# Kernel optimization log

Measured on AMD Instinct MI355X. Metric: run time of the kernel, lower is better.

Reference implementation:

```python
import jax, jax.numpy as jnp
import numpy as np

IN_F, OUT_F, R = 4096, 4096, 16
ALPHA = 32.0
SCALING = ALPHA / R


def setup_inputs() -> dict:
    key = jax.random.key(0)
    kx, kw, ka = jax.random.split(key, 3)
    x = jax.random.normal(kx, (4, 2048, IN_F), dtype=jnp.float32)
    # xavier_normal for weight: std = sqrt(2/(fan_in+fan_out))
    std = float(np.sqrt(2.0 / (IN_F + OUT_F)))
    weight = jax.random.normal(kw, (OUT_F, IN_F), dtype=jnp.float32) * std
    bias = jnp.zeros((OUT_F,), dtype=jnp.float32)
    A = jax.random.normal(ka, (R, IN_F), dtype=jnp.float32) * 0.01
    # B initialized to zeros in the module, but use small random values so the
    # LoRA path is numerically exercised for kernel correctness testing.
    B = jax.random.normal(jax.random.fold_in(key, 7), (OUT_F, R), dtype=jnp.float32) * 0.01
    return {"x": x, "weight": weight, "bias": bias, "A": A, "B": B}


def reference(x, weight, bias, A, B):
    # out = x @ W^T + bias + scaling * ((x @ A^T) @ B^T)
    out = jnp.einsum('bsi,oi->bso', x, weight) + bias
    xa = jnp.einsum('bsi,ri->bsr', x, A)           # [b, s, r] low-rank projection
    out = out + SCALING * jnp.einsum('bsr,or->bso', xa, B)
    return out
```

## Files before the change

kernel.cpp:

```cpp
#include <hip/hip_runtime.h>
#include <hip/hip_bf16.h>
#include <cstdint>
#include <cstddef>


#define IN_F   4096
#define OUT_F  4096
#define MROWS  8192
#define RLORA  16
#define LORA_SCALE 2.0f

#define BM 128
#define BN 128
#define BK 32

typedef __bf16 bf16x8 __attribute__((ext_vector_type(8)));
typedef float  f32x4  __attribute__((ext_vector_type(4)));


__device__ __forceinline__ unsigned short f2bf_rne(float f) {
    union { float f; unsigned u; } v; v.f = f;
    unsigned u = v.u;
    return (unsigned short)((u + 0x7FFFu + ((u >> 16) & 1u)) >> 16);
}

__device__ __forceinline__ void gl_lds16(const unsigned short* g, unsigned short* l) {
    __builtin_amdgcn_global_load_lds(
        (const __attribute__((address_space(1))) unsigned int*)g,
        (__attribute__((address_space(3))) unsigned int*)l,
        16, 0, 0);
}


__global__ void cast_x_kernel(const float* __restrict__ x,
                              unsigned short* __restrict__ xb) {
    int i = blockIdx.x * blockDim.x + threadIdx.x;
    float4 v = ((const float4*)x)[i];
    ushort4 o;
    o.x = f2bf_rne(v.x); o.y = f2bf_rne(v.y);
    o.z = f2bf_rne(v.z); o.w = f2bf_rne(v.w);
    ((ushort4*)xb)[i] = o;
}


__global__ void fold_w_kernel(const float* __restrict__ W,
                              const float* __restrict__ A,
                              const float* __restrict__ B,
                              unsigned short* __restrict__ Wp) {
    int o = blockIdx.x;
    __shared__ float sB[RLORA];
    if (threadIdx.x < RLORA) sB[threadIdx.x] = B[o * RLORA + threadIdx.x];
    __syncthreads();
    const float4* W4  = (const float4*)(W + (size_t)o * IN_F);
    ushort4*      Wp4 = (ushort4*)(Wp + (size_t)o * IN_F);
    for (int i4 = threadIdx.x; i4 < IN_F / 4; i4 += blockDim.x) {
        float4 w = W4[i4];
        float ax = 0.f, ay = 0.f, az = 0.f, aw = 0.f;
        #pragma unroll
        for (int r = 0; r < RLORA; ++r) {
            float4 a = ((const float4*)(A + (size_t)r * IN_F))[i4];
            float s = sB[r];
            ax += s * a.x; ay += s * a.y; az += s * a.z; aw += s * a.w;
        }
        w.x += LORA_SCALE * ax; w.y += LORA_SCALE * ay;
        w.z += LORA_SCALE * az; w.w += LORA_SCALE * aw;
        ushort4 ov;
        ov.x = f2bf_rne(w.x); ov.y = f2bf_rne(w.y);
        ov.z = f2bf_rne(w.z); ov.w = f2bf_rne(w.w);
        Wp4[i4] = ov;
    }
}


__global__ __launch_bounds__(256)
void gemm_bt_bias(const unsigned short* __restrict__ Xb,
                  const unsigned short* __restrict__ Wb,
                  const float* __restrict__ bias,
                  float* __restrict__ out) {
    __shared__ __align__(16) unsigned short As[BM * BK];
    __shared__ __align__(16) unsigned short Bs[BN * BK];

    const int tid  = threadIdx.x;
    const int wave = tid >> 6;
    const int lane = tid & 63;
    const int quad = lane >> 4;
    const int r16  = lane & 15;
    const int wm   = wave >> 1;
    const int wn   = wave & 1;

    const int m0 = blockIdx.y * BM;
    const int n0 = blockIdx.x * BN;

    const int c0   = wave * 128 + lane;
    const int c1   = c0 + 64;
    const int row0 = c0 >> 2, kc0 = c0 & 3;
    const int row1 = c1 >> 2, kc1 = c1 & 3;

    const unsigned short* gA0 = Xb + (size_t)(m0 + row0) * IN_F + kc0 * 8;
    const unsigned short* gA1 = Xb + (size_t)(m0 + row1) * IN_F + kc1 * 8;
    const unsigned short* gB0 = Wb + (size_t)(n0 + row0) * IN_F + kc0 * 8;
    const unsigned short* gB1 = Wb + (size_t)(n0 + row1) * IN_F + kc1 * 8;

    unsigned short* lA0 = As + (wave * 128 +  0) * 8;
    unsigned short* lA1 = As + (wave * 128 + 64) * 8;
    unsigned short* lB0 = Bs + (wave * 128 +  0) * 8;
    unsigned short* lB1 = Bs + (wave * 128 + 64) * 8;

    const unsigned short* pA = As + ((wm * 64 + r16) * BK) + quad * 8;
    const unsigned short* pB = Bs + ((wn * 64 + r16) * BK) + quad * 8;

    f32x4 acc[4][4] = {};

    for (int k0 = 0; k0 < IN_F; k0 += BK) {
        gl_lds16(gA0, lA0);
        gl_lds16(gA1, lA1);
        gl_lds16(gB0, lB0);
        gl_lds16(gB1, lB1);
        gA0 += BK; gA1 += BK; gB0 += BK; gB1 += BK;
        __syncthreads();

        bf16x8 aF[4], bF[4];
        #pragma unroll
        for (int mi = 0; mi < 4; ++mi)
            aF[mi] = *(const bf16x8*)(pA + mi * 16 * BK);
        #pragma unroll
        for (int ni = 0; ni < 4; ++ni)
            bF[ni] = *(const bf16x8*)(pB + ni * 16 * BK);

        #pragma unroll
        for (int mi = 0; mi < 4; ++mi)
            #pragma unroll
            for (int ni = 0; ni < 4; ++ni)
                acc[mi][ni] = __builtin_amdgcn_mfma_f32_16x16x32_bf16(
                    aF[mi], bF[ni], acc[mi][ni], 0, 0, 0);

        __syncthreads();
    }

    float bv[4];
    #pragma unroll
    for (int ni = 0; ni < 4; ++ni)
        bv[ni] = bias[n0 + wn * 64 + ni * 16 + r16];

    #pragma unroll
    for (int mi = 0; mi < 4; ++mi) {
        #pragma unroll
        for (int i = 0; i < 4; ++i) {
            int mg = m0 + wm * 64 + mi * 16 + quad * 4 + i;
            float* orow = out + (size_t)mg * OUT_F + (n0 + wn * 64 + r16);
            #pragma unroll
            for (int ni = 0; ni < 4; ++ni)
                orow[ni * 16] = acc[mi][ni][i] + bv[ni];
        }
    }
}


extern "C" void kernel_launch(void* const* d_in, const int* in_sizes, int n_in,
                              void* d_out, int out_size, void* d_ws, size_t ws_size,
                              hipStream_t stream) {
    const float* x    = (const float*)d_in[0];
    const float* W    = (const float*)d_in[1];
    const float* bias = (const float*)d_in[2];
    const float* A    = (const float*)d_in[3];
    const float* B    = (const float*)d_in[4];
    float* out = (float*)d_out;

    unsigned short* xb = (unsigned short*)d_ws;
    unsigned short* wb = xb + (size_t)MROWS * IN_F;

    cast_x_kernel<<<(MROWS * IN_F) / (4 * 256), 256, 0, stream>>>(x, xb);
    fold_w_kernel<<<OUT_F, 256, 0, stream>>>(W, A, B, wb);

    dim3 grid(OUT_F / BN, MROWS / BM);
    gemm_bt_bias<<<grid, 256, 0, stream>>>(xb, wb, bias, out);
}
```

Measured before the change: 609.8 us.

## Merge prep kernels and remap GEMM tiles for XCD-local L2 reuse

```diff
diff --git a/kernel.cpp b/kernel.cpp
--- a/kernel.cpp
+++ b/kernel.cpp
@@ -14,9 +14,11 @@
 #define BN 128
 #define BK 32
 
+#define CAST_BLOCKS 32768
+#define FOLD_BLOCKS 4096
+
 typedef __bf16 bf16x8 __attribute__((ext_vector_type(8)));
 typedef float  f32x4  __attribute__((ext_vector_type(4)));
-
 
 __device__ __forceinline__ unsigned short f2bf_rne(float f) {
     union { float f; unsigned u; } v; v.f = f;
@@ -32,42 +34,43 @@
 }
 
 
-__global__ void cast_x_kernel(const float* __restrict__ x,
-                              unsigned short* __restrict__ xb) {
-    int i = blockIdx.x * blockDim.x + threadIdx.x;
-    float4 v = ((const float4*)x)[i];
-    ushort4 o;
-    o.x = f2bf_rne(v.x); o.y = f2bf_rne(v.y);
-    o.z = f2bf_rne(v.z); o.w = f2bf_rne(v.w);
-    ((ushort4*)xb)[i] = o;
-}
-
-
-__global__ void fold_w_kernel(const float* __restrict__ W,
-                              const float* __restrict__ A,
-                              const float* __restrict__ B,
-                              unsigned short* __restrict__ Wp) {
-    int o = blockIdx.x;
+__global__ void prep_kernel(const float* __restrict__ x,
+                            const float* __restrict__ W,
+                            const float* __restrict__ A,
+                            const float* __restrict__ B,
+                            unsigned short* __restrict__ xb,
+                            unsigned short* __restrict__ wb) {
     __shared__ float sB[RLORA];
-    if (threadIdx.x < RLORA) sB[threadIdx.x] = B[o * RLORA + threadIdx.x];
-    __syncthreads();
-    const float4* W4  = (const float4*)(W + (size_t)o * IN_F);
-    ushort4*      Wp4 = (ushort4*)(Wp + (size_t)o * IN_F);
-    for (int i4 = threadIdx.x; i4 < IN_F / 4; i4 += blockDim.x) {
-        float4 w = W4[i4];
-        float ax = 0.f, ay = 0.f, az = 0.f, aw = 0.f;
-        #pragma unroll
-        for (int r = 0; r < RLORA; ++r) {
-            float4 a = ((const float4*)(A + (size_t)r * IN_F))[i4];
-            float s = sB[r];
-            ax += s * a.x; ay += s * a.y; az += s * a.z; aw += s * a.w;
+    const int bid = blockIdx.x;
+    if (bid < CAST_BLOCKS) {
+        int i = bid * blockDim.x + threadIdx.x;
+        float4 v = ((const float4*)x)[i];
+        ushort4 o;
+        o.x = f2bf_rne(v.x); o.y = f2bf_rne(v.y);
+        o.z = f2bf_rne(v.z); o.w = f2bf_rne(v.w);
+        ((ushort4*)xb)[i] = o;
+    } else {
+        const int o = bid - CAST_BLOCKS;
+        if (threadIdx.x < RLORA) sB[threadIdx.x] = B[o * RLORA + threadIdx.x];
+        __syncthreads();
+        const float4* W4  = (const float4*)(W + (size_t)o * IN_F);
+        ushort4*      Wp4 = (ushort4*)(wb + (size_t)o * IN_F);
+        for (int i4 = threadIdx.x; i4 < IN_F / 4; i4 += blockDim.x) {
+            float4 w = W4[i4];
+            float ax = 0.f, ay = 0.f, az = 0.f, aw = 0.f;
+            #pragma unroll
+            for (int r = 0; r < RLORA; ++r) {
+                float4 a = ((const float4*)(A + (size_t)r * IN_F))[i4];
+                float s = sB[r];
+                ax += s * a.x; ay += s * a.y; az += s * a.z; aw += s * a.w;
+            }
+            w.x += LORA_SCALE * ax; w.y += LORA_SCALE * ay;
+            w.z += LORA_SCALE * az; w.w += LORA_SCALE * aw;
+            ushort4 ov;
+            ov.x = f2bf_rne(w.x); ov.y = f2bf_rne(w.y);
+            ov.z = f2bf_rne(w.z); ov.w = f2bf_rne(w.w);
+            Wp4[i4] = ov;
         }
-        w.x += LORA_SCALE * ax; w.y += LORA_SCALE * ay;
-        w.z += LORA_SCALE * az; w.w += LORA_SCALE * aw;
-        ushort4 ov;
-        ov.x = f2bf_rne(w.x); ov.y = f2bf_rne(w.y);
-        ov.z = f2bf_rne(w.z); ov.w = f2bf_rne(w.w);
-        Wp4[i4] = ov;
     }
 }
 
@@ -88,8 +91,11 @@
     const int wm   = wave >> 1;
     const int wn   = wave & 1;
 
-    const int m0 = blockIdx.y * BM;
-    const int n0 = blockIdx.x * BN;
+    const int bid = blockIdx.x;
+    const int xcd = bid & 7;
+    const int t   = bid >> 3;
+    const int n0  = ((xcd << 2) | (t & 3)) * BN;
+    const int m0  = (t >> 2) * BM;
 
     const int c0   = wave * 128 + lane;
     const int c1   = c0 + 64;
@@ -169,9 +175,6 @@
     unsigned short* xb = (unsigned short*)d_ws;
     unsigned short* wb = xb + (size_t)MROWS * IN_F;
 
-    cast_x_kernel<<<(MROWS * IN_F) / (4 * 256), 256, 0, stream>>>(x, xb);
-    fold_w_kernel<<<OUT_F, 256, 0, stream>>>(W, A, B, wb);
-
-    dim3 grid(OUT_F / BN, MROWS / BM);
-    gemm_bt_bias<<<grid, 256, 0, stream>>>(xb, wb, bias, out);
+    prep_kernel<<<CAST_BLOCKS + FOLD_BLOCKS, 256, 0, stream>>>(x, W, A, B, xb, wb);
+    gemm_bt_bias<<<2048, 256, 0, stream>>>(xb, wb, bias, out);
 }
```

Result: no change. 603.9 us (-1.0%).
